# Optimization experiments

Measured on AMD Instinct MI355X. Metric: run time of the kernel, lower is better.

The kernel has to match this reference:

```python
import jax, jax.numpy as jnp
import numpy as np

B, L, D = 1, 2048, 768
H, DH = 12, 64  # n_heads, d_head (D // H)
LN_EPS = 1e-5
DEN_EPS = 1e-6


def setup_inputs() -> dict:
    key = jax.random.key(0)
    ks = jax.random.split(key, 11)
    s = 0.02
    return {
        "x": jax.random.normal(ks[0], (B, L, D), dtype=jnp.float32),
        "W_qkv": jax.random.normal(ks[1], (D, 3 * D), dtype=jnp.float32) * s,
        "b_qkv": jnp.zeros((3 * D,), dtype=jnp.float32),
        "W_sem": jax.random.normal(ks[2], (D, 2 * D), dtype=jnp.float32) * s,
        "b_sem": jnp.zeros((2 * D,), dtype=jnp.float32),
        "W_ctx": jax.random.normal(ks[3], (D, 2 * D), dtype=jnp.float32) * s,
        "b_ctx": jnp.zeros((2 * D,), dtype=jnp.float32),
        "W_proj": jax.random.normal(ks[4], (D, D), dtype=jnp.float32) * s,
        "b_proj": jnp.zeros((D,), dtype=jnp.float32),
        "ln_g": jnp.ones((D,), dtype=jnp.float32),
        "ln_b": jnp.zeros((D,), dtype=jnp.float32),
    }


def _heads(t):
    # [B,L,D] -> [B,H,L,DH]
    return t.reshape(B, L, H, DH).transpose(0, 2, 1, 3)


def reference(x, W_qkv, b_qkv, W_sem, b_sem, W_ctx, b_ctx, W_proj, b_proj, ln_g, ln_b):
    # LayerNorm
    mu = jnp.mean(x, axis=-1, keepdims=True)
    var = jnp.mean(jnp.square(x - mu), axis=-1, keepdims=True)
    x_norm = (x - mu) * jax.lax.rsqrt(var + LN_EPS) * ln_g + ln_b

    qkv = x_norm @ W_qkv + b_qkv
    q, k, v = jnp.split(qkv, 3, axis=-1)

    # interference gate from raw x
    sem = x @ W_sem + b_sem
    sem_amp = jax.nn.softplus(sem[..., :D])
    sem_phase = sem[..., D:]
    ctx = x @ W_ctx + b_ctx
    ctx_amp = jax.nn.softplus(ctx[..., :D])
    ctx_phase = ctx[..., D:]
    gate = jax.nn.sigmoid(sem_amp * ctx_amp * jnp.cos(sem_phase - ctx_phase))
    k = k * gate

    q_f = jax.nn.elu(_heads(q)) + 1.0  # [B,H,L,DH]
    k_f = jax.nn.elu(_heads(k)) + 1.0
    v_f = _heads(v)

    # causal linear attention: cumsum of kv outer products along L
    kv = jnp.einsum("bhld,bhle->bhlde", k_f, v_f)  # [B,H,L,DH,DH]
    kv_cum = jnp.cumsum(kv, axis=2)
    out_num = jnp.einsum("bhld,bhlde->bhle", q_f, kv_cum)  # [B,H,L,DH]

    k_cum = jnp.cumsum(k_f, axis=2)
    out_den = jnp.sum(q_f * k_cum, axis=-1, keepdims=True) + DEN_EPS

    attn = (out_num / out_den).transpose(0, 2, 1, 3).reshape(B, L, D)
    return attn @ W_proj + b_proj
```

## Files before the change

kernel.cpp:

```cpp
#include <hip/hip_runtime.h>
#include <math.h>

#define LSEQ 2048
#define DMODEL 768
#define NHEAD 12
#define DHEAD 64
#define NCHUNK 32
#define CSIZE 64
#define NMERGED 5376

typedef unsigned short ushort_t;
typedef __attribute__((ext_vector_type(8))) short short8;
typedef float float4v __attribute__((ext_vector_type(4)));

__device__ __forceinline__ ushort_t f2b(float f) {
    union { float f; unsigned int u; } v; v.f = f;
    unsigned int u = v.u;
    return (ushort_t)((u + 0x7fffu + ((u >> 16) & 1u)) >> 16);
}
__device__ __forceinline__ float b2f(ushort_t u) {
    union { unsigned int u; float f; } v; v.u = ((unsigned int)u) << 16;
    return v.f;
}

__device__ __forceinline__ void gl_lds16(const ushort_t* g, ushort_t* l) {
    __builtin_amdgcn_global_load_lds(
        (const __attribute__((address_space(1))) unsigned int*)g,
        (__attribute__((address_space(3))) unsigned int*)l, 16, 0, 0);
}

__global__ void ln_kernel(const float* __restrict__ x, const float* __restrict__ g,
                          const float* __restrict__ beta, ushort_t* __restrict__ xn,
                          ushort_t* __restrict__ xb) {
    int row = blockIdx.x;
    int tid = threadIdx.x;
    const float* xr = x + (size_t)row * DMODEL;
    float v0 = xr[tid], v1 = xr[tid + 256], v2 = xr[tid + 512];
    __shared__ float red[4];
    __shared__ float bc;
    float s = v0 + v1 + v2;
#pragma unroll
    for (int o = 32; o > 0; o >>= 1) s += __shfl_down(s, o);
    if ((tid & 63) == 0) red[tid >> 6] = s;
    __syncthreads();
    if (tid == 0) bc = (red[0] + red[1] + red[2] + red[3]) * (1.0f / DMODEL);
    __syncthreads();
    float mu = bc;
    float d0 = v0 - mu, d1 = v1 - mu, d2 = v2 - mu;
    float vs = d0 * d0 + d1 * d1 + d2 * d2;
    __syncthreads();
#pragma unroll
    for (int o = 32; o > 0; o >>= 1) vs += __shfl_down(vs, o);
    if ((tid & 63) == 0) red[tid >> 6] = vs;
    __syncthreads();
    if (tid == 0) bc = rsqrtf((red[0] + red[1] + red[2] + red[3]) * (1.0f / DMODEL) + 1e-5f);
    __syncthreads();
    float r = bc;
    ushort_t* xo = xn + (size_t)row * DMODEL;
    ushort_t* xc = xb + (size_t)row * DMODEL;
    xo[tid]       = f2b(d0 * r * g[tid]       + beta[tid]);
    xo[tid + 256] = f2b(d1 * r * g[tid + 256] + beta[tid + 256]);
    xo[tid + 512] = f2b(d2 * r * g[tid + 512] + beta[tid + 512]);
    xc[tid]       = f2b(v0);
    xc[tid + 256] = f2b(v1);
    xc[tid + 512] = f2b(v2);
}

__global__ void transpose_all_kernel(const float* __restrict__ Wq, const float* __restrict__ Ws,
                                     const float* __restrict__ Wc, ushort_t* __restrict__ Tm,
                                     const float* __restrict__ Wp, ushort_t* __restrict__ Tp) {
    const float* W; ushort_t* Wt; int N;
    switch (blockIdx.z) {
        case 0: W = Wq; Wt = Tm;                        N = 2304; break;
        case 1: W = Ws; Wt = Tm + (size_t)2304 * 768;   N = 1536; break;
        case 2: W = Wc; Wt = Tm + (size_t)3840 * 768;   N = 1536; break;
        default: W = Wp; Wt = Tp;                       N = 768;  break;
    }
    int nbase = blockIdx.x * 32;
    if (nbase >= N) return;
    __shared__ float tile[32][33];
    int tid = threadIdx.x;
    int tr = tid >> 5, tc = tid & 31;
    int kbase = blockIdx.y * 32;
#pragma unroll
    for (int p = 0; p < 4; p++) {
        int r = p * 8 + tr;
        tile[r][tc] = W[(size_t)(kbase + r) * N + nbase + tc];
    }
    __syncthreads();
#pragma unroll
    for (int p = 0; p < 4; p++) {
        int r = p * 8 + tr;
        Wt[(size_t)(nbase + r) * 768 + kbase + tc] = f2b(tile[tc][r]);
    }
}

__global__ __launch_bounds__(256) void gemm_merged_kernel(
    const ushort_t* __restrict__ Axn, const ushort_t* __restrict__ Axb,
    const ushort_t* __restrict__ Bt,
    const float* __restrict__ b_qkv, const float* __restrict__ b_sem,
    const float* __restrict__ b_ctx, float* __restrict__ C) {
    const int K = 768, N = NMERGED;
    __shared__ ushort_t As[128 * 32];
    __shared__ ushort_t Bs[128 * 32];
    int tid = threadIdx.x;
    int wave = tid >> 6, lane = tid & 63;
    int wm = (wave >> 1) * 64, wn = (wave & 1) * 64;
    int quad = lane >> 4, l16 = lane & 15;
    int m0 = blockIdx.y * 128, n0 = blockIdx.x * 128;
    const ushort_t* A = (n0 < 2304) ? Axn : Axb;
    const float* bias = (n0 < 2304) ? (b_qkv + n0) : (n0 < 3840 ? (b_sem + n0 - 2304) : (b_ctx + n0 - 3840));

    int r0 = tid >> 2;
    int kc = (tid & 3) * 8;
    const ushort_t* Ag0 = A + (size_t)(m0 + r0) * K + kc;
    const ushort_t* Ag1 = A + (size_t)(m0 + 64 + r0) * K + kc;
    const ushort_t* Bg0 = Bt + (size_t)(n0 + r0) * K + kc;
    const ushort_t* Bg1 = Bt + (size_t)(n0 + 64 + r0) * K + kc;
    ushort_t* Al0 = &As[(wave * 64) * 8];
    ushort_t* Al1 = &As[(256 + wave * 64) * 8];
    ushort_t* Bl0 = &Bs[(wave * 64) * 8];
    ushort_t* Bl1 = &Bs[(256 + wave * 64) * 8];

    float4v acc[4][4];
#pragma unroll
    for (int i = 0; i < 4; i++)
#pragma unroll
        for (int j = 0; j < 4; j++)
#pragma unroll
            for (int r = 0; r < 4; r++) acc[i][j][r] = 0.0f;

    for (int k0 = 0; k0 < K; k0 += 32) {
        gl_lds16(Ag0 + k0, Al0);
        gl_lds16(Ag1 + k0, Al1);
        gl_lds16(Bg0 + k0, Bl0);
        gl_lds16(Bg1 + k0, Bl1);
        __syncthreads();
        short8 af[4], bf[4];
#pragma unroll
        for (int i = 0; i < 4; i++) af[i] = *(const short8*)&As[(wm + i * 16 + l16) * 32 + quad * 8];
#pragma unroll
        for (int j = 0; j < 4; j++) bf[j] = *(const short8*)&Bs[(wn + j * 16 + l16) * 32 + quad * 8];
#pragma unroll
        for (int i = 0; i < 4; i++)
#pragma unroll
            for (int j = 0; j < 4; j++)
                acc[i][j] = __builtin_amdgcn_mfma_f32_16x16x32_bf16(af[i], bf[j], acc[i][j], 0, 0, 0);
        __syncthreads();
    }
#pragma unroll
    for (int i = 0; i < 4; i++) {
#pragma unroll
        for (int j = 0; j < 4; j++) {
            int colb = wn + j * 16 + l16;
            float bv = bias[colb];
#pragma unroll
            for (int r = 0; r < 4; r++) {
                int row = m0 + wm + i * 16 + quad * 4 + r;
                C[(size_t)row * N + n0 + colb] = acc[i][j][r] + bv;
            }
        }
    }
}

__global__ __launch_bounds__(256) void gemm_64_kernel(
    const ushort_t* __restrict__ A, const ushort_t* __restrict__ Bt,
    const float* __restrict__ bias, float* __restrict__ C,
    int N, int K) {
    __shared__ ushort_t As[64 * 32];
    __shared__ ushort_t Bs[64 * 32];
    int tid = threadIdx.x;
    int wave = tid >> 6, lane = tid & 63;
    int wm = (wave >> 1) * 32, wn = (wave & 1) * 32;
    int quad = lane >> 4, l16 = lane & 15;
    int m0 = blockIdx.y * 64, n0 = blockIdx.x * 64;

    int r0 = tid >> 2;
    int kc = (tid & 3) * 8;
    const ushort_t* Ag = A + (size_t)(m0 + r0) * K + kc;
    const ushort_t* Bg = Bt + (size_t)(n0 + r0) * K + kc;
    ushort_t* Al = &As[(wave * 16) * 32];
    ushort_t* Bl = &Bs[(wave * 16) * 32];

    float4v acc[2][2];
#pragma unroll
    for (int i = 0; i < 2; i++)
#pragma unroll
        for (int j = 0; j < 2; j++)
#pragma unroll
            for (int r = 0; r < 4; r++) acc[i][j][r] = 0.0f;

    for (int k0 = 0; k0 < K; k0 += 32) {
        gl_lds16(Ag + k0, Al);
        gl_lds16(Bg + k0, Bl);
        __syncthreads();
        short8 af[2], bf[2];
#pragma unroll
        for (int i = 0; i < 2; i++) af[i] = *(const short8*)&As[(wm + i * 16 + l16) * 32 + quad * 8];
#pragma unroll
        for (int j = 0; j < 2; j++) bf[j] = *(const short8*)&Bs[(wn + j * 16 + l16) * 32 + quad * 8];
#pragma unroll
        for (int i = 0; i < 2; i++)
#pragma unroll
            for (int j = 0; j < 2; j++)
                acc[i][j] = __builtin_amdgcn_mfma_f32_16x16x32_bf16(af[i], bf[j], acc[i][j], 0, 0, 0);
        __syncthreads();
    }
#pragma unroll
    for (int i = 0; i < 2; i++) {
#pragma unroll
        for (int j = 0; j < 2; j++) {
            int col = n0 + wn + j * 16 + l16;
            float bv = bias[col];
#pragma unroll
            for (int r = 0; r < 4; r++) {
                int row = m0 + wm + i * 16 + quad * 4 + r;
                C[(size_t)row * N + col] = acc[i][j][r] + bv;
            }
        }
    }
}

__device__ __forceinline__ float softplus_f(float x) {
    return (x > 15.f) ? x : log1pf(expf(x));
}

__global__ void gate_feat_kernel(const float* __restrict__ qsc,
                                 ushort_t* __restrict__ qf, ushort_t* __restrict__ kf) {
    int t = blockIdx.x * 256 + threadIdx.x;
    int l = t / 192, d = (t - l * 192) * 4;
    size_t base = (size_t)l * NMERGED;
    float sa[4], sp[4], ca[4], cp[4], q[4], k[4];
    *(float4*)sa = *(const float4*)&qsc[base + 2304 + d];
    *(float4*)sp = *(const float4*)&qsc[base + 3072 + d];
    *(float4*)ca = *(const float4*)&qsc[base + 3840 + d];
    *(float4*)cp = *(const float4*)&qsc[base + 4608 + d];
    *(float4*)q  = *(const float4*)&qsc[base + d];
    *(float4*)k  = *(const float4*)&qsc[base + 768 + d];
    ushort_t qo[4], ko[4];
#pragma unroll
    for (int j = 0; j < 4; j++) {
        float amp = softplus_f(sa[j]) * softplus_f(ca[j]);
        float tt = amp * cosf(sp[j] - cp[j]);
        float gate = 1.0f / (1.0f + expf(-tt));
        float kv = k[j] * gate;
        float qv = q[j];
        qo[j] = f2b((qv > 0.f) ? qv + 1.0f : expf(qv));
        ko[j] = f2b((kv > 0.f) ? kv + 1.0f : expf(kv));
    }
    size_t o = (size_t)l * DMODEL + d;
    *(uint2*)&qf[o] = *(uint2*)qo;
    *(uint2*)&kf[o] = *(uint2*)ko;
}

__global__ void chunk_sum_kernel(const ushort_t* __restrict__ kf, const float* __restrict__ qsc,
                                 float* __restrict__ S) {
    int h = blockIdx.x % NHEAD;
    int c = blockIdx.x / NHEAD;
    __shared__ float ks[64][64];
    __shared__ float vs[64][64];
    int tid = threadIdx.x;
#pragma unroll
    for (int it = 0; it < 4; it++) {
        int r = it * 16 + (tid >> 4);
        int cc = (tid & 15) * 4;
        int lg = c * 64 + r;
        ushort_t kt[4];
        *(uint2*)kt = *(const uint2*)&kf[(size_t)lg * DMODEL + h * DHEAD + cc];
        ks[r][cc + 0] = b2f(kt[0]); ks[r][cc + 1] = b2f(kt[1]);
        ks[r][cc + 2] = b2f(kt[2]); ks[r][cc + 3] = b2f(kt[3]);
        *(float4*)&vs[r][cc] = *(const float4*)&qsc[(size_t)lg * NMERGED + 1536 + h * DHEAD + cc];
    }
    __syncthreads();
    int d = tid >> 2;
    int e0 = (tid & 3) * 16;
    float acc[16] = {};
    float ksum = 0.f;
    for (int l = 0; l < 64; l++) {
        float kd = ks[l][d];
        ksum += kd;
#pragma unroll
        for (int u = 0; u < 16; u++) acc[u] += kd * vs[l][e0 + u];
    }
    float* Sp = S + ((size_t)(h * NCHUNK + c)) * 4160;
#pragma unroll
    for (int u = 0; u < 16; u++) Sp[d * 64 + e0 + u] = acc[u];
    if ((tid & 3) == 0) Sp[4096 + d] = ksum;
}

__global__ void prefix_kernel(float* __restrict__ S) {
    int h = blockIdx.x;
    int i = blockIdx.y * 256 + threadIdx.x;
    if (i >= 4160) return;
    float run = 0.f;
    for (int c = 0; c < NCHUNK; c++) {
        size_t off = ((size_t)(h * NCHUNK + c)) * 4160 + i;
        float v = S[off];
        S[off] = run;
        run += v;
    }
}

__global__ void attn_out_kernel(const ushort_t* __restrict__ qf, const ushort_t* __restrict__ kfb,
                                const float* __restrict__ qsc, const float* __restrict__ P,
                                ushort_t* __restrict__ attn) {
    int h = blockIdx.x % NHEAD;
    int c = blockIdx.x / NHEAD;
    __shared__ float qs[64][64];
    __shared__ float b1[64][64];
    __shared__ float b2[64][64];
    int tid = threadIdx.x;
    const size_t pbase = ((size_t)(h * NCHUNK + c)) * 4160;
#pragma unroll
    for (int it = 0; it < 4; it++) {
        int r = it * 16 + (tid >> 4);
        int cc = (tid & 15) * 4;
        int lg = c * 64 + r;
        ushort_t qt[4];
        *(uint2*)qt = *(const uint2*)&qf[(size_t)lg * DMODEL + h * DHEAD + cc];
        qs[r][cc + 0] = b2f(qt[0]); qs[r][cc + 1] = b2f(qt[1]);
        qs[r][cc + 2] = b2f(qt[2]); qs[r][cc + 3] = b2f(qt[3]);
        *(float4*)&b1[r][cc] = *(const float4*)&P[pbase + r * 64 + cc];
    }
    if (tid < 16) *(float4*)&b2[0][tid * 4] = *(const float4*)&P[pbase + 4096 + tid * 4];
    __syncthreads();
    int l = tid >> 2;
    int e0 = (tid & 3) * 16;
    float qreg[64];
#pragma unroll
    for (int d = 0; d < 64; d++) qreg[d] = qs[l][d];
    float num[16] = {};
    float den = 1e-6f;
    for (int d = 0; d < 64; d++) {
        float qd = qreg[d];
        den += qd * b2[0][d];
#pragma unroll
        for (int u = 0; u < 16; u++) num[u] += qd * b1[d][e0 + u];
    }
    __syncthreads();
#pragma unroll
    for (int it = 0; it < 4; it++) {
        int r = it * 16 + (tid >> 4);
        int cc = (tid & 15) * 4;
        int lg = c * 64 + r;
        ushort_t kt[4];
        *(uint2*)kt = *(const uint2*)&kfb[(size_t)lg * DMODEL + h * DHEAD + cc];
        b1[r][cc + 0] = b2f(kt[0]); b1[r][cc + 1] = b2f(kt[1]);
        b1[r][cc + 2] = b2f(kt[2]); b1[r][cc + 3] = b2f(kt[3]);
        b2[r][cc + 0] = 0.f;
        *(float4*)&b2[r][cc] = *(const float4*)&qsc[(size_t)lg * NMERGED + 1536 + h * DHEAD + cc];
    }
    __syncthreads();
    for (int j = 0; j <= l; j++) {
        float a = 0.f;
#pragma unroll
        for (int d = 0; d < 64; d++) a += qreg[d] * b1[j][d];
        den += a;
#pragma unroll
        for (int u = 0; u < 16; u++) num[u] += a * b2[j][e0 + u];
    }
    float inv = 1.0f / den;
    ushort_t ob[16];
#pragma unroll
    for (int u = 0; u < 16; u++) ob[u] = f2b(num[u] * inv);
    ushort_t* op = attn + (size_t)(c * 64 + l) * DMODEL + h * DHEAD + e0;
    *(uint4*)&op[0] = *(uint4*)&ob[0];
    *(uint4*)&op[8] = *(uint4*)&ob[8];
}

extern "C" void kernel_launch(void* const* d_in, const int* in_sizes, int n_in,
                              void* d_out, int out_size, void* d_ws, size_t ws_size,
                              hipStream_t stream) {
    const float* x      = (const float*)d_in[0];
    const float* W_qkv  = (const float*)d_in[1];
    const float* b_qkv  = (const float*)d_in[2];
    const float* W_sem  = (const float*)d_in[3];
    const float* b_sem  = (const float*)d_in[4];
    const float* W_ctx  = (const float*)d_in[5];
    const float* b_ctx  = (const float*)d_in[6];
    const float* W_proj = (const float*)d_in[7];
    const float* b_proj = (const float*)d_in[8];
    const float* ln_g   = (const float*)d_in[9];
    const float* ln_b   = (const float*)d_in[10];
    float* out = (float*)d_out;
    float* ws  = (float*)d_ws;

    ushort_t* Wt_merged = (ushort_t*)(ws);
    ushort_t* Wt_proj   = (ushort_t*)(ws + 2064384);
    ushort_t* xb        = (ushort_t*)(ws + 2359296);
    ushort_t* xnb       = (ushort_t*)(ws + 3145728);
    float*    qsc       = ws + 3932160;
    ushort_t* qf        = (ushort_t*)(ws + 14942208);
    ushort_t* kf        = (ushort_t*)(ws + 3145728);
    float*    S         = ws;
    ushort_t* attnb     = (ushort_t*)(ws + 2359296);

    ln_kernel<<<LSEQ, 256, 0, stream>>>(x, ln_g, ln_b, xnb, xb);
    transpose_all_kernel<<<dim3(72, 24, 4), 256, 0, stream>>>(W_qkv, W_sem, W_ctx, Wt_merged,
                                                              W_proj, Wt_proj);

    gemm_merged_kernel<<<dim3(NMERGED / 128, LSEQ / 128), 256, 0, stream>>>(
        xnb, xb, Wt_merged, b_qkv, b_sem, b_ctx, qsc);

    gate_feat_kernel<<<(LSEQ * DMODEL / 4) / 256, 256, 0, stream>>>(qsc, qf, kf);
    chunk_sum_kernel<<<NHEAD * NCHUNK, 256, 0, stream>>>(kf, qsc, S);
    prefix_kernel<<<dim3(NHEAD, 17), 256, 0, stream>>>(S);
    attn_out_kernel<<<NHEAD * NCHUNK, 256, 0, stream>>>(qf, kf, qsc, S, attnb);

    gemm_64_kernel<<<dim3(768 / 64, LSEQ / 64), 256, 0, stream>>>(attnb, Wt_proj, b_proj, out, 768, 768);
}
```

Before: 196.4 us.

## Move chunked linear attention onto bf16 MFMA with bf16 V and prefix state

Rewrites the per-chunk KV-sum and the intra/inter-chunk attention kernels to use bf16 MFMA tiles instead of scalar FP32 FMA loops. The merged GEMM now writes V directly as bf16 into a separate buffer, and the prefix scan emits a bf16 copy of the prefix state plus an FP32 key-sum vector. This cuts the scalar ALU work and the FP32 memory traffic in the attention stage. The cost is extra rounding of the scores, V and the prefix state to bf16, plus reshuffled workspace aliasing.

```diff
diff --git a/kernel.cpp b/kernel.cpp
--- a/kernel.cpp
+++ b/kernel.cpp
@@ -6,7 +6,6 @@
 #define NHEAD 12
 #define DHEAD 64
 #define NCHUNK 32
-#define CSIZE 64
 #define NMERGED 5376
 
 typedef unsigned short ushort_t;
@@ -99,7 +98,8 @@
     const ushort_t* __restrict__ Axn, const ushort_t* __restrict__ Axb,
     const ushort_t* __restrict__ Bt,
     const float* __restrict__ b_qkv, const float* __restrict__ b_sem,
-    const float* __restrict__ b_ctx, float* __restrict__ C) {
+    const float* __restrict__ b_ctx, float* __restrict__ C,
+    ushort_t* __restrict__ vb) {
     const int K = 768, N = NMERGED;
     __shared__ ushort_t As[128 * 32];
     __shared__ ushort_t Bs[128 * 32];
@@ -148,6 +148,7 @@
                 acc[i][j] = __builtin_amdgcn_mfma_f32_16x16x32_bf16(af[i], bf[j], acc[i][j], 0, 0, 0);
         __syncthreads();
     }
+    bool is_v = (n0 >= 1536 && n0 < 2304);
 #pragma unroll
     for (int i = 0; i < 4; i++) {
 #pragma unroll
@@ -157,7 +158,12 @@
 #pragma unroll
             for (int r = 0; r < 4; r++) {
                 int row = m0 + wm + i * 16 + quad * 4 + r;
-                C[(size_t)row * N + n0 + colb] = acc[i][j][r] + bv;
+                float o = acc[i][j][r] + bv;
+                if (is_v) {
+                    vb[(size_t)row * DMODEL + (n0 - 1536) + colb] = f2b(o);
+                } else {
+                    C[(size_t)row * N + n0 + colb] = o;
+                }
             }
         }
     }
@@ -253,119 +259,204 @@
     *(uint2*)&kf[o] = *(uint2*)ko;
 }
 
-__global__ void chunk_sum_kernel(const ushort_t* __restrict__ kf, const float* __restrict__ qsc,
-                                 float* __restrict__ S) {
+__global__ __launch_bounds__(256) void chunk_sum_mfma(const ushort_t* __restrict__ kf,
+                                                      const ushort_t* __restrict__ vb,
+                                                      float* __restrict__ S) {
     int h = blockIdx.x % NHEAD;
     int c = blockIdx.x / NHEAD;
-    __shared__ float ks[64][64];
-    __shared__ float vs[64][64];
+    __shared__ ushort_t Kt[64 * 72];
+    __shared__ ushort_t Vt[64 * 72];
     int tid = threadIdx.x;
+    const size_t hb = (size_t)h * DHEAD;
 #pragma unroll
     for (int it = 0; it < 4; it++) {
         int r = it * 16 + (tid >> 4);
         int cc = (tid & 15) * 4;
         int lg = c * 64 + r;
-        ushort_t kt[4];
-        *(uint2*)kt = *(const uint2*)&kf[(size_t)lg * DMODEL + h * DHEAD + cc];
-        ks[r][cc + 0] = b2f(kt[0]); ks[r][cc + 1] = b2f(kt[1]);
-        ks[r][cc + 2] = b2f(kt[2]); ks[r][cc + 3] = b2f(kt[3]);
-        *(float4*)&vs[r][cc] = *(const float4*)&qsc[(size_t)lg * NMERGED + 1536 + h * DHEAD + cc];
-    }
-    __syncthreads();
-    int d = tid >> 2;
-    int e0 = (tid & 3) * 16;
-    float acc[16] = {};
-    float ksum = 0.f;
-    for (int l = 0; l < 64; l++) {
-        float kd = ks[l][d];
-        ksum += kd;
-#pragma unroll
-        for (int u = 0; u < 16; u++) acc[u] += kd * vs[l][e0 + u];
-    }
-    float* Sp = S + ((size_t)(h * NCHUNK + c)) * 4160;
-#pragma unroll
-    for (int u = 0; u < 16; u++) Sp[d * 64 + e0 + u] = acc[u];
-    if ((tid & 3) == 0) Sp[4096 + d] = ksum;
-}
-
-__global__ void prefix_kernel(float* __restrict__ S) {
+        ushort_t kt4[4], vt4[4];
+        *(uint2*)kt4 = *(const uint2*)&kf[(size_t)lg * DMODEL + hb + cc];
+        *(uint2*)vt4 = *(const uint2*)&vb[(size_t)lg * DMODEL + hb + cc];
+#pragma unroll
+        for (int i2 = 0; i2 < 4; i2++) {
+            Kt[(cc + i2) * 72 + r] = kt4[i2];
+            Vt[(cc + i2) * 72 + r] = vt4[i2];
+        }
+    }
+    __syncthreads();
+    int wave = tid >> 6, lane = tid & 63, quad = lane >> 4, l16 = lane & 15;
+    int wm = wave * 16;
+    float4v acc[4];
+#pragma unroll
+    for (int jt = 0; jt < 4; jt++)
+#pragma unroll
+        for (int r = 0; r < 4; r++) acc[jt][r] = 0.0f;
+#pragma unroll
+    for (int ks = 0; ks < 2; ks++) {
+        short8 af = *(const short8*)&Kt[(wm + l16) * 72 + ks * 32 + quad * 8];
+#pragma unroll
+        for (int jt = 0; jt < 4; jt++) {
+            short8 bf = *(const short8*)&Vt[(jt * 16 + l16) * 72 + ks * 32 + quad * 8];
+            acc[jt] = __builtin_amdgcn_mfma_f32_16x16x32_bf16(af, bf, acc[jt], 0, 0, 0);
+        }
+    }
+    float* Sp = S + (size_t)(h * NCHUNK + c) * 4160;
+#pragma unroll
+    for (int jt = 0; jt < 4; jt++) {
+        float4 o;
+        o.x = acc[jt][0]; o.y = acc[jt][1]; o.z = acc[jt][2]; o.w = acc[jt][3];
+        *(float4*)&Sp[(jt * 16 + l16) * 64 + wm + quad * 4] = o;
+    }
+    if (tid < 64) {
+        float s = 0.f;
+#pragma unroll
+        for (int g = 0; g < 8; g++) {
+            short8 kv8 = *(const short8*)&Kt[tid * 72 + g * 8];
+#pragma unroll
+            for (int i2 = 0; i2 < 8; i2++) s += b2f(((ushort_t*)&kv8)[i2]);
+        }
+        Sp[4096 + tid] = s;
+    }
+}
+
+__global__ void prefix_kernel(const float* __restrict__ S, ushort_t* __restrict__ Pb,
+                              float* __restrict__ kpf) {
     int h = blockIdx.x;
     int i = blockIdx.y * 256 + threadIdx.x;
     if (i >= 4160) return;
+    float v[NCHUNK];
+    size_t base = (size_t)h * NCHUNK * 4160 + i;
+#pragma unroll
+    for (int c2 = 0; c2 < NCHUNK; c2++) v[c2] = S[base + (size_t)c2 * 4160];
     float run = 0.f;
-    for (int c = 0; c < NCHUNK; c++) {
-        size_t off = ((size_t)(h * NCHUNK + c)) * 4160 + i;
-        float v = S[off];
-        S[off] = run;
-        run += v;
-    }
-}
-
-__global__ void attn_out_kernel(const ushort_t* __restrict__ qf, const ushort_t* __restrict__ kfb,
-                                const float* __restrict__ qsc, const float* __restrict__ P,
-                                ushort_t* __restrict__ attn) {
+    if (i < 4096) {
+        size_t pb = (size_t)h * NCHUNK * 4096 + i;
+#pragma unroll
+        for (int c2 = 0; c2 < NCHUNK; c2++) {
+            Pb[pb + (size_t)c2 * 4096] = f2b(run);
+            run += v[c2];
+        }
+    } else {
+        size_t kb = (size_t)h * NCHUNK * 64 + (i - 4096);
+#pragma unroll
+        for (int c2 = 0; c2 < NCHUNK; c2++) {
+            kpf[kb + (size_t)c2 * 64] = run;
+            run += v[c2];
+        }
+    }
+}
+
+__global__ __launch_bounds__(256) void attn_out_mfma(const ushort_t* __restrict__ qf,
+                                                     const ushort_t* __restrict__ kf,
+                                                     const ushort_t* __restrict__ vb,
+                                                     const ushort_t* __restrict__ Pb,
+                                                     const float* __restrict__ kpf,
+                                                     ushort_t* __restrict__ attn) {
     int h = blockIdx.x % NHEAD;
     int c = blockIdx.x / NHEAD;
-    __shared__ float qs[64][64];
-    __shared__ float b1[64][64];
-    __shared__ float b2[64][64];
+    __shared__ ushort_t Qs[64 * 72];
+    __shared__ ushort_t Ks[64 * 72];
+    __shared__ ushort_t Pt[64 * 72];
+    __shared__ ushort_t Vt[64 * 72];
+    __shared__ float Sc[64 * 68];
+    __shared__ float kpl[64];
+    __shared__ float denp[4][64];
+    __shared__ float dnl[64];
     int tid = threadIdx.x;
-    const size_t pbase = ((size_t)(h * NCHUNK + c)) * 4160;
+    const size_t hb = (size_t)h * DHEAD;
+    const size_t pcb = (size_t)(h * NCHUNK + c);
+#pragma unroll
+    for (int it = 0; it < 2; it++) {
+        int chunk = it * 256 + tid;
+        int r = chunk >> 3, c8 = (chunk & 7) * 8;
+        int lg = c * 64 + r;
+        *(uint4*)&Qs[r * 72 + c8] = *(const uint4*)&qf[(size_t)lg * DMODEL + hb + c8];
+        *(uint4*)&Ks[r * 72 + c8] = *(const uint4*)&kf[(size_t)lg * DMODEL + hb + c8];
+        *(uint4*)&Pt[r * 72 + c8] = *(const uint4*)&Pb[pcb * 4096 + r * 64 + c8];
+    }
 #pragma unroll
     for (int it = 0; it < 4; it++) {
         int r = it * 16 + (tid >> 4);
         int cc = (tid & 15) * 4;
         int lg = c * 64 + r;
-        ushort_t qt[4];
-        *(uint2*)qt = *(const uint2*)&qf[(size_t)lg * DMODEL + h * DHEAD + cc];
-        qs[r][cc + 0] = b2f(qt[0]); qs[r][cc + 1] = b2f(qt[1]);
-        qs[r][cc + 2] = b2f(qt[2]); qs[r][cc + 3] = b2f(qt[3]);
-        *(float4*)&b1[r][cc] = *(const float4*)&P[pbase + r * 64 + cc];
-    }
-    if (tid < 16) *(float4*)&b2[0][tid * 4] = *(const float4*)&P[pbase + 4096 + tid * 4];
-    __syncthreads();
-    int l = tid >> 2;
-    int e0 = (tid & 3) * 16;
-    float qreg[64];
-#pragma unroll
-    for (int d = 0; d < 64; d++) qreg[d] = qs[l][d];
-    float num[16] = {};
-    float den = 1e-6f;
-    for (int d = 0; d < 64; d++) {
-        float qd = qreg[d];
-        den += qd * b2[0][d];
-#pragma unroll
-        for (int u = 0; u < 16; u++) num[u] += qd * b1[d][e0 + u];
-    }
-    __syncthreads();
-#pragma unroll
-    for (int it = 0; it < 4; it++) {
-        int r = it * 16 + (tid >> 4);
-        int cc = (tid & 15) * 4;
-        int lg = c * 64 + r;
-        ushort_t kt[4];
-        *(uint2*)kt = *(const uint2*)&kfb[(size_t)lg * DMODEL + h * DHEAD + cc];
-        b1[r][cc + 0] = b2f(kt[0]); b1[r][cc + 1] = b2f(kt[1]);
-        b1[r][cc + 2] = b2f(kt[2]); b1[r][cc + 3] = b2f(kt[3]);
-        b2[r][cc + 0] = 0.f;
-        *(float4*)&b2[r][cc] = *(const float4*)&qsc[(size_t)lg * NMERGED + 1536 + h * DHEAD + cc];
-    }
-    __syncthreads();
-    for (int j = 0; j <= l; j++) {
-        float a = 0.f;
-#pragma unroll
-        for (int d = 0; d < 64; d++) a += qreg[d] * b1[j][d];
-        den += a;
-#pragma unroll
-        for (int u = 0; u < 16; u++) num[u] += a * b2[j][e0 + u];
-    }
-    float inv = 1.0f / den;
-    ushort_t ob[16];
-#pragma unroll
-    for (int u = 0; u < 16; u++) ob[u] = f2b(num[u] * inv);
-    ushort_t* op = attn + (size_t)(c * 64 + l) * DMODEL + h * DHEAD + e0;
-    *(uint4*)&op[0] = *(uint4*)&ob[0];
-    *(uint4*)&op[8] = *(uint4*)&ob[8];
+        ushort_t vt4[4];
+        *(uint2*)vt4 = *(const uint2*)&vb[(size_t)lg * DMODEL + hb + cc];
+#pragma unroll
+        for (int i2 = 0; i2 < 4; i2++) Vt[(cc + i2) * 72 + r] = vt4[i2];
+    }
+    if (tid < 64) kpl[tid] = kpf[pcb * 64 + tid];
+    __syncthreads();
+    int wave = tid >> 6, lane = tid & 63, quad = lane >> 4, l16 = lane & 15;
+    int wm = wave * 16;
+    float4v s_acc[4], n_acc[4];
+#pragma unroll
+    for (int jt = 0; jt < 4; jt++)
+#pragma unroll
+        for (int r = 0; r < 4; r++) { s_acc[jt][r] = 0.0f; n_acc[jt][r] = 0.0f; }
+#pragma unroll
+    for (int ks = 0; ks < 2; ks++) {
+        short8 aq = *(const short8*)&Qs[(wm + l16) * 72 + ks * 32 + quad * 8];
+#pragma unroll
+        for (int jt = 0; jt < 4; jt++) {
+            short8 bk = *(const short8*)&Ks[(jt * 16 + l16) * 72 + ks * 32 + quad * 8];
+            short8 bp = *(const short8*)&Pt[(jt * 16 + l16) * 72 + ks * 32 + quad * 8];
+            s_acc[jt] = __builtin_amdgcn_mfma_f32_16x16x32_bf16(aq, bk, s_acc[jt], 0, 0, 0);
+            n_acc[jt] = __builtin_amdgcn_mfma_f32_16x16x32_bf16(aq, bp, n_acc[jt], 0, 0, 0);
+        }
+    }
+#pragma unroll
+    for (int jt = 0; jt < 4; jt++)
+#pragma unroll
+        for (int r = 0; r < 4; r++)
+            Sc[(wm + quad * 4 + r) * 68 + jt * 16 + l16] = s_acc[jt][r];
+    __syncthreads();
+    {
+        int l = tid & 63, part = tid >> 6;
+        float s = 0.f;
+#pragma unroll
+        for (int jj = 0; jj < 16; jj++) {
+            int j = part * 16 + jj;
+            float v = Sc[l * 68 + j];
+            s += (j <= l) ? v : 0.f;
+        }
+#pragma unroll
+        for (int dd = 0; dd < 16; dd++) {
+            int d = part * 16 + dd;
+            s += b2f(Qs[l * 72 + d]) * kpl[d];
+        }
+        denp[part][l] = s;
+    }
+    __syncthreads();
+    if (tid < 64) dnl[tid] = denp[0][tid] + denp[1][tid] + denp[2][tid] + denp[3][tid] + 1e-6f;
+    __syncthreads();
+#pragma unroll
+    for (int ks = 0; ks < 2; ks++) {
+        int m = wm + l16;
+        float sv[8];
+        *(float4*)&sv[0] = *(const float4*)&Sc[m * 68 + ks * 32 + quad * 8];
+        *(float4*)&sv[4] = *(const float4*)&Sc[m * 68 + ks * 32 + quad * 8 + 4];
+        ushort_t am[8];
+#pragma unroll
+        for (int i2 = 0; i2 < 8; i2++) {
+            int j = ks * 32 + quad * 8 + i2;
+            am[i2] = (j <= m) ? f2b(sv[i2]) : (ushort_t)0;
+        }
+        short8 af = *(short8*)am;
+#pragma unroll
+        for (int jt = 0; jt < 4; jt++) {
+            short8 bv = *(const short8*)&Vt[(jt * 16 + l16) * 72 + ks * 32 + quad * 8];
+            n_acc[jt] = __builtin_amdgcn_mfma_f32_16x16x32_bf16(af, bv, n_acc[jt], 0, 0, 0);
+        }
+    }
+#pragma unroll
+    for (int jt = 0; jt < 4; jt++) {
+        int e = jt * 16 + l16;
+#pragma unroll
+        for (int r = 0; r < 4; r++) {
+            int l = wm + quad * 4 + r;
+            float o = n_acc[jt][r] / dnl[l];
+            attn[(size_t)(c * 64 + l) * DMODEL + hb + e] = f2b(o);
+        }
+    }
 }
 
 extern "C" void kernel_launch(void* const* d_in, const int* in_sizes, int n_in,
@@ -390,22 +481,25 @@
     ushort_t* xb        = (ushort_t*)(ws + 2359296);
     ushort_t* xnb       = (ushort_t*)(ws + 3145728);
     float*    qsc       = ws + 3932160;
-    ushort_t* qf        = (ushort_t*)(ws + 14942208);
+    ushort_t* vb        = (ushort_t*)(ws + 14942208);
+    ushort_t* qf        = (ushort_t*)(ws + 2359296);
     ushort_t* kf        = (ushort_t*)(ws + 3145728);
     float*    S         = ws;
-    ushort_t* attnb     = (ushort_t*)(ws + 2359296);
+    ushort_t* Pb        = (ushort_t*)(ws + 3932160);
+    float*    kpf       = ws + 4718592;
+    ushort_t* attnb     = (ushort_t*)(ws);
 
     ln_kernel<<<LSEQ, 256, 0, stream>>>(x, ln_g, ln_b, xnb, xb);
     transpose_all_kernel<<<dim3(72, 24, 4), 256, 0, stream>>>(W_qkv, W_sem, W_ctx, Wt_merged,
                                                               W_proj, Wt_proj);
 
     gemm_merged_kernel<<<dim3(NMERGED / 128, LSEQ / 128), 256, 0, stream>>>(
-        xnb, xb, Wt_merged, b_qkv, b_sem, b_ctx, qsc);
+        xnb, xb, Wt_merged, b_qkv, b_sem, b_ctx, qsc, vb);
 
     gate_feat_kernel<<<(LSEQ * DMODEL / 4) / 256, 256, 0, stream>>>(qsc, qf, kf);
-    chunk_sum_kernel<<<NHEAD * NCHUNK, 256, 0, stream>>>(kf, qsc, S);
-    prefix_kernel<<<dim3(NHEAD, 17), 256, 0, stream>>>(S);
-    attn_out_kernel<<<NHEAD * NCHUNK, 256, 0, stream>>>(qf, kf, qsc, S, attnb);
+    chunk_sum_mfma<<<NHEAD * NCHUNK, 256, 0, stream>>>(kf, vb, S);
+    prefix_kernel<<<dim3(NHEAD, 17), 256, 0, stream>>>(S, Pb, kpf);
+    attn_out_mfma<<<NHEAD * NCHUNK, 256, 0, stream>>>(qf, kf, vb, Pb, kpf, attnb);
 
     gemm_64_kernel<<<dim3(768 / 64, LSEQ / 64), 256, 0, stream>>>(attnb, Wt_proj, b_proj, out, 768, 768);
 }
```

Result: faster. 163.4 us (-16.8%).
